# Kernel optimization log

Measured on AMD Instinct MI355X. Metric: run time of the kernel, lower is better.

Reference implementation:

```python
import jax, jax.numpy as jnp
import numpy as np

N_NODES = 50000
N_EDGES = 800000
N_GRAPHS = 512
IN_DIM, HID_DIM, EMB_DIM = 128, 256, 128
EPS = 1e-5


def setup_inputs() -> dict:
    key = jax.random.key(0)
    ks = jax.random.split(key, 12)
    x = jax.random.normal(ks[0], (N_NODES, IN_DIM), dtype=jnp.float32)
    edge_index = jax.random.randint(ks[1], (2, N_EDGES), 0, N_NODES, dtype=jnp.int32)
    batch = jnp.sort(jax.random.randint(ks[2], (N_NODES,), 0, N_GRAPHS, dtype=jnp.int32))
    s1 = 1.0 / np.sqrt(IN_DIM)
    s2 = 1.0 / np.sqrt(HID_DIM)
    return {
        "x": x,
        "edge_index": edge_index,
        "batch": batch,
        "W1": jax.random.uniform(ks[3], (IN_DIM, HID_DIM), jnp.float32, -s1, s1),
        "b1": jnp.zeros((HID_DIM,), jnp.float32),
        "gamma1": jnp.ones((HID_DIM,), jnp.float32),
        "beta1": jnp.zeros((HID_DIM,), jnp.float32),
        "W2": jax.random.uniform(ks[4], (HID_DIM, EMB_DIM), jnp.float32, -s2, s2),
        "b2": jnp.zeros((EMB_DIM,), jnp.float32),
        "gamma2": jnp.ones((EMB_DIM,), jnp.float32),
        "beta2": jnp.zeros((EMB_DIM,), jnp.float32),
    }


def _gcn_conv(x, W, b, src, dst, n_nodes):
    # PyG GCNConv: h = xW; aggregate with sym-normalized adjacency incl. self-loops; + bias
    h = x @ W  # [N, D]
    ones = jnp.ones(src.shape[0], dtype=h.dtype)
    deg = jax.ops.segment_sum(ones, dst, num_segments=n_nodes) + 1.0  # self-loop
    dinv = jax.lax.rsqrt(deg)
    norm = dinv[src] * dinv[dst]  # [E]
    msg = h[src] * norm[:, None]  # gather + scale  [E, D]
    agg = jax.ops.segment_sum(msg, dst, num_segments=n_nodes)
    agg = agg + h * (1.0 / deg)[:, None]  # self-loop contribution (norm = 1/deg)
    return agg + b


def _batchnorm(h, gamma, beta):
    mean = jnp.mean(h, axis=0)
    var = jnp.mean(jnp.square(h - mean), axis=0)  # biased, training mode
    return gamma * (h - mean) * jax.lax.rsqrt(var + EPS) + beta


def reference(x, edge_index, batch, W1, b1, gamma1, beta1, W2, b2, gamma2, beta2):
    src, dst = edge_index[0], edge_index[1]
    n = x.shape[0]
    h = _gcn_conv(x, W1, b1, src, dst, n)
    h = _batchnorm(jax.nn.relu(h), gamma1, beta1)
    h = _gcn_conv(h, W2, b2, src, dst, n)
    h = _batchnorm(jax.nn.relu(h), gamma2, beta2)
    return jax.ops.segment_max(h, batch, num_segments=N_GRAPHS)
```

## Files before the change

### kernel.cpp

```cpp
#include <hip/hip_runtime.h>
#include <math.h>

#define N_NODES 50000
#define N_EDGES 800000
#define N_GRAPHS 512
#define IN_DIM 128
#define HID_DIM 256
#define EMB_DIM 128
#define EPS 1e-5f
#define ELLW 64
#define NGROUP 8
#define GROUPN 6250
#define BLK_PER_GROUP 256
#define EPB ((N_EDGES + BLK_PER_GROUP - 1) / BLK_PER_GROUP)
#define F2B_N (N_NODES * IN_DIM / 4)
#define F2B_BLOCKS ((F2B_N + 255) / 256)
#define TW1_BLOCKS ((HID_DIM * IN_DIM + 255) / 256)
#define DINV_BLOCKS ((N_NODES + 255) / 256)

typedef __attribute__((ext_vector_type(8))) short bf16x8;
typedef __attribute__((ext_vector_type(4))) float f32x4;

static __device__ __forceinline__ unsigned short f2b(float f) {
    unsigned u = __float_as_uint(f);
    return (unsigned short)((u + 0x7fffu + ((u >> 16) & 1u)) >> 16);
}
static __device__ __forceinline__ float b2f(unsigned short h) {
    return __uint_as_float(((unsigned)h) << 16);
}

__global__ void __launch_bounds__(256) scatter_xcd(const int* __restrict__ src,
                                                   const int* __restrict__ dst,
                                                   int* __restrict__ fill,
                                                   int* __restrict__ col) {
    int b = blockIdx.x;
    int g = b & 7;
    int bs = b >> 3;
    int lo = g * GROUPN;
    int hi = lo + GROUPN;
    int e_end = min((bs + 1) * EPB, N_EDGES);
    for (int e = bs * EPB + threadIdx.x; e < e_end; e += 256) {
        int d = dst[e];
        if (d >= lo && d < hi) {
            int pos = atomicAdd(&fill[d], 1);
            pos = min(pos, ELLW - 1);
            col[(d << 6) + pos] = src[e];
        }
    }
}

__global__ void convert_kernel(const float* __restrict__ x, unsigned short* __restrict__ xbf,
                               const float* __restrict__ W1, unsigned short* __restrict__ W1t,
                               const int* __restrict__ fill, float* __restrict__ dinv) {
    int b = blockIdx.x;
    if (b < F2B_BLOCKS) {
        int i = b * 256 + threadIdx.x;
        if (i < F2B_N) {
            float4 v = ((const float4*)x)[i];
            ushort4 o;
            o.x = f2b(v.x); o.y = f2b(v.y); o.z = f2b(v.z); o.w = f2b(v.w);
            ((ushort4*)xbf)[i] = o;
        }
    } else if (b < F2B_BLOCKS + TW1_BLOCKS) {
        int j = (b - F2B_BLOCKS) * 256 + threadIdx.x;
        if (j < HID_DIM * IN_DIM) {
            int n = j >> 7;
            int k = j & 127;
            W1t[j] = f2b(W1[k * HID_DIM + n]);
        }
    } else {
        int v = (b - F2B_BLOCKS - TW1_BLOCKS) * 256 + threadIdx.x;
        if (v < N_NODES) dinv[v] = rsqrtf((float)(min(fill[v], ELLW) + 1));
    }
}

static __device__ __forceinline__ void acc8(float* acc, uint4 r, float w) {
    const unsigned* u = (const unsigned*)&r;
#pragma unroll
    for (int k = 0; k < 4; ++k) {
        float lo = __uint_as_float((u[k] & 0xFFFFu) << 16);
        float hi = __uint_as_float(u[k] & 0xFFFF0000u);
        acc[2 * k]     += w * lo;
        acc[2 * k + 1] += w * hi;
    }
}

template <bool RELU, bool OUT_BF, bool BIAS>
__global__ void __launch_bounds__(256) aggw_kernel(const unsigned short* __restrict__ h,
                                                   const float* __restrict__ dinv,
                                                   const int* __restrict__ deg,
                                                   const int* __restrict__ col,
                                                   const float* __restrict__ bias,
                                                   void* __restrict__ y) {
    int tid = threadIdx.x;
    int lane = tid & 63;
    int wid = tid >> 6;
    int v = blockIdx.x * 4 + wid;
    int g = lane >> 4;
    int p = lane & 15;

    int beg = v << 6;
    int end = beg + min(deg[v], ELLW);
    float acc[8] = {};

    for (int e = beg; e < end; e += 16) {
        int i0 = e + g, i1 = e + 4 + g, i2 = e + 8 + g, i3 = e + 12 + g;
        int c0 = min(i0, end - 1), c1 = min(i1, end - 1);
        int c2 = min(i2, end - 1), c3 = min(i3, end - 1);
        int u0 = col[c0], u1 = col[c1], u2 = col[c2], u3 = col[c3];
        float w0 = (i0 < end) ? dinv[u0] : 0.f;
        float w1 = (i1 < end) ? dinv[u1] : 0.f;
        float w2 = (i2 < end) ? dinv[u2] : 0.f;
        float w3 = (i3 < end) ? dinv[u3] : 0.f;
        uint4 d0 = *(const uint4*)(h + (size_t)u0 * 128 + p * 8);
        uint4 d1 = *(const uint4*)(h + (size_t)u1 * 128 + p * 8);
        uint4 d2 = *(const uint4*)(h + (size_t)u2 * 128 + p * 8);
        uint4 d3 = *(const uint4*)(h + (size_t)u3 * 128 + p * 8);
        acc8(acc, d0, w0);
        acc8(acc, d1, w1);
        acc8(acc, d2, w2);
        acc8(acc, d3, w3);
    }

#pragma unroll
    for (int k = 0; k < 8; ++k) {
        float a = acc[k];
        a += __shfl_xor(a, 16, 64);
        a += __shfl_xor(a, 32, 64);
        acc[k] = a;
    }

    if (g == 0) {
        uint4 selfr = *(const uint4*)(h + (size_t)v * 128 + p * 8);
        const unsigned* su = (const unsigned*)&selfr;
        float dv = dinv[v];
        float dv2 = dv * dv;
        float o[8];
#pragma unroll
        for (int k = 0; k < 4; ++k) {
            float lo = __uint_as_float((su[k] & 0xFFFFu) << 16);
            float hi = __uint_as_float(su[k] & 0xFFFF0000u);
            o[2 * k]     = dv * acc[2 * k]     + lo * dv2;
            o[2 * k + 1] = dv * acc[2 * k + 1] + hi * dv2;
        }
        if (BIAS) {
            float4 bv0 = *(const float4*)&bias[p * 8];
            float4 bv1 = *(const float4*)&bias[p * 8 + 4];
            o[0] += bv0.x; o[1] += bv0.y; o[2] += bv0.z; o[3] += bv0.w;
            o[4] += bv1.x; o[5] += bv1.y; o[6] += bv1.z; o[7] += bv1.w;
        }
        if (RELU) {
#pragma unroll
            for (int k = 0; k < 8; ++k) o[k] = fmaxf(o[k], 0.f);
        }
        if (OUT_BF) {
            uint4 packed;
            unsigned* pu = (unsigned*)&packed;
#pragma unroll
            for (int k = 0; k < 4; ++k)
                pu[k] = (unsigned)f2b(o[2 * k]) | ((unsigned)f2b(o[2 * k + 1]) << 16);
            *(uint4*)((unsigned short*)y + (size_t)v * 128 + p * 8) = packed;
        } else {
            float* yf = (float*)y + (size_t)v * 128 + p * 8;
            *(float4*)yf = make_float4(o[0], o[1], o[2], o[3]);
            *(float4*)(yf + 4) = make_float4(o[4], o[5], o[6], o[7]);
        }
    }
}

template <bool RELU, bool STATS>
__global__ void __launch_bounds__(256) mfma_gemm_kernel(const unsigned short* __restrict__ A,
                                                        const unsigned short* __restrict__ Bt,
                                                        const float* __restrict__ bias,
                                                        unsigned short* __restrict__ C,
                                                        float* __restrict__ sum,
                                                        float* __restrict__ sumsq,
                                                        int M, int N, int K) {
    const int LDT = 40;
    __shared__ unsigned short As[64 * LDT];
    __shared__ unsigned short Bs[128 * LDT];
    int tid = threadIdx.x;
    int bm = blockIdx.x * 64;
    int bn = blockIdx.y * 128;
    int lr = tid >> 2;
    int lc = (tid & 3) * 8;
    int lane = tid & 63;
    int w = tid >> 6;
    int wc = w * 32;
    int l15 = lane & 15, q = lane >> 4;

    f32x4 acc[4][2] = {};
    bool arow_ok = (bm + lr) < M;
    const unsigned short* Aptr = A + (size_t)(bm + lr) * K + lc;
    const unsigned short* B0 = Bt + (size_t)(bn + lr) * K + lc;
    const unsigned short* B1 = Bt + (size_t)(bn + lr + 64) * K + lc;

    for (int k0 = 0; k0 < K; k0 += 32) {
        uint4 av = arow_ok ? *(const uint4*)(Aptr + k0) : make_uint4(0u, 0u, 0u, 0u);
        uint4 b0v = *(const uint4*)(B0 + k0);
        uint4 b1v = *(const uint4*)(B1 + k0);
        *(uint4*)&As[lr * LDT + lc] = av;
        *(uint4*)&Bs[lr * LDT + lc] = b0v;
        *(uint4*)&Bs[(lr + 64) * LDT + lc] = b1v;
        __syncthreads();
        bf16x8 af[4], bf[2];
#pragma unroll
        for (int mi = 0; mi < 4; ++mi)
            af[mi] = *(const bf16x8*)&As[(mi * 16 + l15) * LDT + q * 8];
#pragma unroll
        for (int ni = 0; ni < 2; ++ni)
            bf[ni] = *(const bf16x8*)&Bs[(wc + ni * 16 + l15) * LDT + q * 8];
#pragma unroll
        for (int mi = 0; mi < 4; ++mi)
#pragma unroll
            for (int ni = 0; ni < 2; ++ni)
                acc[mi][ni] = __builtin_amdgcn_mfma_f32_16x16x32_bf16(af[mi], bf[ni], acc[mi][ni], 0, 0, 0);
        __syncthreads();
    }

    float s[2] = {0.f, 0.f}, sq[2] = {0.f, 0.f};
#pragma unroll
    for (int ni = 0; ni < 2; ++ni) {
        int colc = bn + wc + ni * 16 + l15;
        float bv = bias ? bias[colc] : 0.f;
#pragma unroll
        for (int mi = 0; mi < 4; ++mi) {
#pragma unroll
            for (int r = 0; r < 4; ++r) {
                int row = bm + mi * 16 + q * 4 + r;
                bool ok = row < M;
                float vv = acc[mi][ni][r] + bv;
                if (RELU) vv = fmaxf(vv, 0.f);
                unsigned short us = f2b(vv);
                if (ok) C[(size_t)row * N + colc] = us;
                if (STATS) {
                    float xr = ok ? b2f(us) : 0.f;
                    s[ni] += xr;
                    sq[ni] += xr * xr;
                }
            }
        }
    }
    if (STATS) {
#pragma unroll
        for (int ni = 0; ni < 2; ++ni) {
            float a = s[ni], b = sq[ni];
            a += __shfl_xor(a, 16, 64); a += __shfl_xor(a, 32, 64);
            b += __shfl_xor(b, 16, 64); b += __shfl_xor(b, 32, 64);
            if (q == 0) {
                int colc = bn + wc + ni * 16 + l15;
                atomicAdd(&sum[colc], a);
                atomicAdd(&sumsq[colc], b);
            }
        }
    }
}

template <int C, bool BF>
__global__ void __launch_bounds__(256) stats_fast(const void* __restrict__ yv,
                                                  float* __restrict__ sum,
                                                  float* __restrict__ sumsq) {
    constexpr int VEC = BF ? 8 : 4;
    constexpr int NCHUNK = C / VEC;
    constexpr int ROWS = 256 / NCHUNK;
    constexpr int STRIDE = 256 * ROWS;
    __shared__ float sp[256 * VEC];
    __shared__ float qp[256 * VEC];
    int t = threadIdx.x;
    int j = t & (NCHUNK - 1);
    float s[VEC], q[VEC];
#pragma unroll
    for (int k = 0; k < VEC; ++k) { s[k] = 0.f; q[k] = 0.f; }

    const char* base = (const char*)yv + (size_t)j * 16;
    auto body = [&](int v) {
        uint4 raw = *(const uint4*)(base + (size_t)v * (C * (BF ? 2 : 4)));
        float x[VEC];
        if (BF) {
            const unsigned* u = (const unsigned*)&raw;
#pragma unroll
            for (int k = 0; k < 4; ++k) {
                x[2 * k]     = __uint_as_float((u[k] & 0xFFFFu) << 16);
                x[2 * k + 1] = __uint_as_float(u[k] & 0xFFFF0000u);
            }
        } else {
            const float* f = (const float*)&raw;
#pragma unroll
            for (int k = 0; k < VEC; ++k) x[k] = f[k];
        }
#pragma unroll
        for (int k = 0; k < VEC; ++k) { s[k] += x[k]; q[k] += x[k] * x[k]; }
    };

    int v = blockIdx.x * ROWS + (t >> 5);
    for (; v + 3 * STRIDE < N_NODES; v += 4 * STRIDE) {
        body(v); body(v + STRIDE); body(v + 2 * STRIDE); body(v + 3 * STRIDE);
    }
    for (; v < N_NODES; v += STRIDE) body(v);

#pragma unroll
    for (int k = 0; k < VEC; ++k) { sp[t * VEC + k] = s[k]; qp[t * VEC + k] = q[k]; }
    __syncthreads();
    if (t < C) {
        float ss = 0.f, qq = 0.f;
#pragma unroll
        for (int rr = 0; rr < ROWS; ++rr) {
            ss += sp[rr * (NCHUNK * VEC) + t];
            qq += qp[rr * (NCHUNK * VEC) + t];
        }
        atomicAdd(&sum[t], ss);
        atomicAdd(&sumsq[t], qq);
    }
}

__global__ void prep2_kernel(const float* __restrict__ sum1, const float* __restrict__ sumsq1,
                             const float* __restrict__ gamma1, const float* __restrict__ beta1,
                             const float* __restrict__ W2, unsigned short* __restrict__ W2pt,
                             float* __restrict__ bc2) {
    __shared__ float a1s[HID_DIM], s1s[HID_DIM];
    int t = threadIdx.x;
    {
        float m = sum1[t] * (1.f / N_NODES);
        float var = sumsq1[t] * (1.f / N_NODES) - m * m;
        float a = gamma1[t] * rsqrtf(var + EPS);
        a1s[t] = a;
        s1s[t] = beta1[t] - m * a;
    }
    __syncthreads();
    if (t < EMB_DIM) {
        float bacc = 0.f;
        for (int k = 0; k < HID_DIM; ++k) {
            float w = W2[k * EMB_DIM + t];
            W2pt[t * HID_DIM + k] = f2b(a1s[k] * w);
            bacc += s1s[k] * w;
        }
        bc2[t] = bacc;
    }
}

__global__ void __launch_bounds__(128) segmax_kernel(const float* __restrict__ y,
                                                     const float* __restrict__ sum2,
                                                     const float* __restrict__ sumsq2,
                                                     const float* __restrict__ gamma2,
                                                     const float* __restrict__ beta2,
                                                     const int* __restrict__ batch,
                                                     float* __restrict__ out) {
    __shared__ int sh[2];
    int g = blockIdx.x;
    int c = threadIdx.x;
    float mch = sum2[c] * (1.f / N_NODES);
    float var = sumsq2[c] * (1.f / N_NODES) - mch * mch;
    float ac = gamma2[c] * rsqrtf(var + EPS);
    float sc = beta2[c] - mch * ac;
    if (threadIdx.x == 0) {
        int lo = 0, hi = N_NODES;
        while (lo < hi) { int mid = (lo + hi) >> 1; if (batch[mid] < g) lo = mid + 1; else hi = mid; }
        sh[0] = lo;
        hi = N_NODES;
        while (lo < hi) { int mid = (lo + hi) >> 1; if (batch[mid] < g + 1) lo = mid + 1; else hi = mid; }
        sh[1] = lo;
    }
    __syncthreads();
    int beg = sh[0], end = sh[1];
    float m = -INFINITY;
    for (int v = beg; v < end; ++v) {
        m = fmaxf(m, fmaf(ac, y[(size_t)v * EMB_DIM + c], sc));
    }
    out[(size_t)g * EMB_DIM + c] = m;
}

extern "C" void kernel_launch(void* const* d_in, const int* in_sizes, int n_in,
                              void* d_out, int out_size, void* d_ws, size_t ws_size,
                              hipStream_t stream) {
    const float* x      = (const float*)d_in[0];
    const int*   ei     = (const int*)d_in[1];
    const int*   batch  = (const int*)d_in[2];
    const float* W1     = (const float*)d_in[3];
    const float* b1     = (const float*)d_in[4];
    const float* gamma1 = (const float*)d_in[5];
    const float* beta1  = (const float*)d_in[6];
    const float* W2     = (const float*)d_in[7];
    const float* b2     = (const float*)d_in[8];
    const float* gamma2 = (const float*)d_in[9];
    const float* beta2  = (const float*)d_in[10];
    float* out = (float*)d_out;

    char* ws = (char*)d_ws;
    size_t off = 0;
    auto alloc = [&](size_t bytes) -> char* {
        char* p = ws + off;
        off = (off + bytes + 255) & ~(size_t)255;
        return p;
    };
    int*   fill   = (int*)alloc((size_t)N_NODES * 4);
    float* stats  = (float*)alloc(1024 * 4);
    size_t zbytes = off;
    int*   col    = (int*)alloc((size_t)N_NODES * ELLW * 4);
    float* dinv   = (float*)alloc((size_t)N_NODES * 4);
    float* bc2    = (float*)alloc((size_t)EMB_DIM * 4);
    unsigned short* W1t  = (unsigned short*)alloc((size_t)HID_DIM * IN_DIM * 2);
    unsigned short* W2pt = (unsigned short*)alloc((size_t)HID_DIM * EMB_DIM * 2);
    unsigned short* xbf  = (unsigned short*)alloc((size_t)N_NODES * IN_DIM * 2);
    unsigned short* axbf = (unsigned short*)alloc((size_t)N_NODES * IN_DIM * 2);
    unsigned short* y1bf = (unsigned short*)alloc((size_t)N_NODES * HID_DIM * 2);
    unsigned short* gbf  = (unsigned short*)alloc((size_t)N_NODES * EMB_DIM * 2);
    float* y2 = (float*)xbf;
    (void)ws_size; (void)in_sizes; (void)n_in; (void)out_size;

    const int* src  = ei;
    const int* dstp = ei + N_EDGES;

    hipMemsetAsync(ws, 0, zbytes, stream);

    scatter_xcd<<<NGROUP * BLK_PER_GROUP, 256, 0, stream>>>(src, dstp, fill, col);
    convert_kernel<<<F2B_BLOCKS + TW1_BLOCKS + DINV_BLOCKS, 256, 0, stream>>>(
        x, xbf, W1, W1t, fill, dinv);

    aggw_kernel<false, true, false><<<N_NODES / 4, 256, 0, stream>>>(xbf, dinv, fill, col, nullptr, axbf);
    dim3 g1((N_NODES + 63) / 64, HID_DIM / 128);
    mfma_gemm_kernel<true, true><<<g1, 256, 0, stream>>>(axbf, W1t, b1, y1bf,
                                                         stats, stats + 256,
                                                         N_NODES, HID_DIM, IN_DIM);

    prep2_kernel<<<1, 256, 0, stream>>>(stats, stats + 256, gamma1, beta1, W2, W2pt, bc2);

    dim3 g2((N_NODES + 63) / 64, EMB_DIM / 128);
    mfma_gemm_kernel<false, false><<<g2, 256, 0, stream>>>(y1bf, W2pt, bc2, gbf,
                                                           nullptr, nullptr,
                                                           N_NODES, EMB_DIM, HID_DIM);
    aggw_kernel<true, false, true><<<N_NODES / 4, 256, 0, stream>>>(gbf, dinv, fill, col, b2, y2);
    stats_fast<EMB_DIM, false><<<256, 256, 0, stream>>>(y2, stats + 512, stats + 640);

    segmax_kernel<<<N_GRAPHS, 128, 0, stream>>>(y2, stats + 512, stats + 640,
                                                gamma2, beta2, batch, out);
}
```

Measured before the change: 319.0 us.

## Keep whole weight matrix resident in LDS and A rows in registers for GEMMs

Replaces the tiled 64x128 MFMA GEMM, which staged A and B tiles through shared memory every 32-wide K step behind two barriers, with a kernel that loads the full transposed weight matrix once per block into LDS in MFMA-fragment order. Each wave keeps its 32 A rows entirely in registers and loops over all output column tiles. This removes per-K-step syncs and the re-reads of A across column blocks. In exchange it uses 64 KB of LDS per block, which limits occupancy, and many registers for the A fragments. Output stores remain scalar 2-byte writes.

```diff
diff --git a/kernel.cpp b/kernel.cpp
--- a/kernel.cpp
+++ b/kernel.cpp
@@ -17,6 +17,7 @@
 #define F2B_BLOCKS ((F2B_N + 255) / 256)
 #define TW1_BLOCKS ((HID_DIM * IN_DIM + 255) / 256)
 #define DINV_BLOCKS ((N_NODES + 255) / 256)
+#define GEMM_BLOCKS ((N_NODES + 127) / 128)
 
 typedef __attribute__((ext_vector_type(8))) short bf16x8;
 typedef __attribute__((ext_vector_type(4))) float f32x4;
@@ -168,89 +169,90 @@
     }
 }
 
-template <bool RELU, bool STATS>
-__global__ void __launch_bounds__(256) mfma_gemm_kernel(const unsigned short* __restrict__ A,
-                                                        const unsigned short* __restrict__ Bt,
-                                                        const float* __restrict__ bias,
-                                                        unsigned short* __restrict__ C,
-                                                        float* __restrict__ sum,
-                                                        float* __restrict__ sumsq,
-                                                        int M, int N, int K) {
-    const int LDT = 40;
-    __shared__ unsigned short As[64 * LDT];
-    __shared__ unsigned short Bs[128 * LDT];
+template <bool RELU, bool STATS, int N, int K>
+__global__ void __launch_bounds__(256) gemm_wres(const unsigned short* __restrict__ A,
+                                                 const unsigned short* __restrict__ Bt,
+                                                 const float* __restrict__ bias,
+                                                 unsigned short* __restrict__ C,
+                                                 float* __restrict__ sum,
+                                                 float* __restrict__ sumsq,
+                                                 int M) {
+    constexpr int NT = N / 16;
+    constexpr int KT = K / 32;
+    __shared__ unsigned short Blds[N * K];
     int tid = threadIdx.x;
-    int bm = blockIdx.x * 64;
-    int bn = blockIdx.y * 128;
-    int lr = tid >> 2;
-    int lc = (tid & 3) * 8;
     int lane = tid & 63;
     int w = tid >> 6;
-    int wc = w * 32;
     int l15 = lane & 15, q = lane >> 4;
 
-    f32x4 acc[4][2] = {};
-    bool arow_ok = (bm + lr) < M;
-    const unsigned short* Aptr = A + (size_t)(bm + lr) * K + lc;
-    const unsigned short* B0 = Bt + (size_t)(bn + lr) * K + lc;
-    const unsigned short* B1 = Bt + (size_t)(bn + lr + 64) * K + lc;
-
-    for (int k0 = 0; k0 < K; k0 += 32) {
-        uint4 av = arow_ok ? *(const uint4*)(Aptr + k0) : make_uint4(0u, 0u, 0u, 0u);
-        uint4 b0v = *(const uint4*)(B0 + k0);
-        uint4 b1v = *(const uint4*)(B1 + k0);
-        *(uint4*)&As[lr * LDT + lc] = av;
-        *(uint4*)&Bs[lr * LDT + lc] = b0v;
-        *(uint4*)&Bs[(lr + 64) * LDT + lc] = b1v;
-        __syncthreads();
-        bf16x8 af[4], bf[2];
-#pragma unroll
-        for (int mi = 0; mi < 4; ++mi)
-            af[mi] = *(const bf16x8*)&As[(mi * 16 + l15) * LDT + q * 8];
-#pragma unroll
-        for (int ni = 0; ni < 2; ++ni)
-            bf[ni] = *(const bf16x8*)&Bs[(wc + ni * 16 + l15) * LDT + q * 8];
-#pragma unroll
-        for (int mi = 0; mi < 4; ++mi)
-#pragma unroll
-            for (int ni = 0; ni < 2; ++ni)
-                acc[mi][ni] = __builtin_amdgcn_mfma_f32_16x16x32_bf16(af[mi], bf[ni], acc[mi][ni], 0, 0, 0);
-        __syncthreads();
-    }
-
-    float s[2] = {0.f, 0.f}, sq[2] = {0.f, 0.f};
-#pragma unroll
-    for (int ni = 0; ni < 2; ++ni) {
-        int colc = bn + wc + ni * 16 + l15;
-        float bv = bias ? bias[colc] : 0.f;
-#pragma unroll
-        for (int mi = 0; mi < 4; ++mi) {
-#pragma unroll
-            for (int r = 0; r < 4; ++r) {
-                int row = bm + mi * 16 + q * 4 + r;
-                bool ok = row < M;
-                float vv = acc[mi][ni][r] + bv;
-                if (RELU) vv = fmaxf(vv, 0.f);
-                unsigned short us = f2b(vv);
-                if (ok) C[(size_t)row * N + colc] = us;
-                if (STATS) {
-                    float xr = ok ? b2f(us) : 0.f;
-                    s[ni] += xr;
-                    sq[ni] += xr * xr;
+    for (int c = tid; c < N * K / 8; c += 256) {
+        int f = c >> 6;
+        int l = c & 63;
+        int nt = f / KT, kk = f - nt * KT;
+        int sl15 = l & 15, sq = l >> 4;
+        uint4 v = *(const uint4*)(Bt + (size_t)(nt * 16 + sl15) * K + kk * 32 + sq * 8);
+        *(uint4*)&Blds[(size_t)c * 8] = v;
+    }
+    __syncthreads();
+
+    int mbase = blockIdx.x * 128 + w * 32;
+    int ar0 = mbase + l15;
+    int ar1 = mbase + 16 + l15;
+    int ac0 = min(ar0, M - 1);
+    int ac1 = min(ar1, M - 1);
+
+    uint4 areg0[KT], areg1[KT];
+#pragma unroll
+    for (int kk = 0; kk < KT; ++kk) {
+        areg0[kk] = *(const uint4*)(A + (size_t)ac0 * K + kk * 32 + q * 8);
+        areg1[kk] = *(const uint4*)(A + (size_t)ac1 * K + kk * 32 + q * 8);
+    }
+
+    for (int nt = 0; nt < NT; nt += 2) {
+        f32x4 acc00 = {}, acc01 = {}, acc10 = {}, acc11 = {};
+#pragma unroll
+        for (int kk = 0; kk < KT; ++kk) {
+            bf16x8 b0 = *(const bf16x8*)&Blds[(size_t)(((nt + 0) * KT + kk) * 64 + lane) * 8];
+            bf16x8 b1 = *(const bf16x8*)&Blds[(size_t)(((nt + 1) * KT + kk) * 64 + lane) * 8];
+            bf16x8 a0 = *(const bf16x8*)&areg0[kk];
+            bf16x8 a1 = *(const bf16x8*)&areg1[kk];
+            acc00 = __builtin_amdgcn_mfma_f32_16x16x32_bf16(a0, b0, acc00, 0, 0, 0);
+            acc10 = __builtin_amdgcn_mfma_f32_16x16x32_bf16(a1, b0, acc10, 0, 0, 0);
+            acc01 = __builtin_amdgcn_mfma_f32_16x16x32_bf16(a0, b1, acc01, 0, 0, 0);
+            acc11 = __builtin_amdgcn_mfma_f32_16x16x32_bf16(a1, b1, acc11, 0, 0, 0);
+        }
+#pragma unroll
+        for (int ni = 0; ni < 2; ++ni) {
+            int colc = (nt + ni) * 16 + l15;
+            float bv = bias ? bias[colc] : 0.f;
+            float s = 0.f, sq2 = 0.f;
+#pragma unroll
+            for (int mi = 0; mi < 2; ++mi) {
+                const f32x4& acc = (mi == 0) ? (ni == 0 ? acc00 : acc01)
+                                             : (ni == 0 ? acc10 : acc11);
+                int rbase = mbase + mi * 16 + q * 4;
+#pragma unroll
+                for (int r = 0; r < 4; ++r) {
+                    int row = rbase + r;
+                    bool ok = row < M;
+                    float vv = acc[r] + bv;
+                    if (RELU) vv = fmaxf(vv, 0.f);
+                    unsigned short us = f2b(vv);
+                    if (ok) C[(size_t)row * N + colc] = us;
+                    if (STATS) {
+                        float xr = ok ? b2f(us) : 0.f;
+                        s += xr;
+                        sq2 += xr * xr;
+                    }
                 }
             }
-        }
-    }
-    if (STATS) {
-#pragma unroll
-        for (int ni = 0; ni < 2; ++ni) {
-            float a = s[ni], b = sq[ni];
-            a += __shfl_xor(a, 16, 64); a += __shfl_xor(a, 32, 64);
-            b += __shfl_xor(b, 16, 64); b += __shfl_xor(b, 32, 64);
-            if (q == 0) {
-                int colc = bn + wc + ni * 16 + l15;
-                atomicAdd(&sum[colc], a);
-                atomicAdd(&sumsq[colc], b);
+            if (STATS) {
+                s += __shfl_xor(s, 16, 64);  s += __shfl_xor(s, 32, 64);
+                sq2 += __shfl_xor(sq2, 16, 64); sq2 += __shfl_xor(sq2, 32, 64);
+                if (q == 0) {
+                    atomicAdd(&sum[colc], s);
+                    atomicAdd(&sumsq[colc], sq2);
+                }
             }
         }
     }
@@ -417,17 +419,13 @@
         x, xbf, W1, W1t, fill, dinv);
 
     aggw_kernel<false, true, false><<<N_NODES / 4, 256, 0, stream>>>(xbf, dinv, fill, col, nullptr, axbf);
-    dim3 g1((N_NODES + 63) / 64, HID_DIM / 128);
-    mfma_gemm_kernel<true, true><<<g1, 256, 0, stream>>>(axbf, W1t, b1, y1bf,
-                                                         stats, stats + 256,
-                                                         N_NODES, HID_DIM, IN_DIM);
+    gemm_wres<true, true, HID_DIM, IN_DIM><<<GEMM_BLOCKS, 256, 0, stream>>>(
+        axbf, W1t, b1, y1bf, stats, stats + 256, N_NODES);
 
     prep2_kernel<<<1, 256, 0, stream>>>(stats, stats + 256, gamma1, beta1, W2, W2pt, bc2);
 
-    dim3 g2((N_NODES + 63) / 64, EMB_DIM / 128);
-    mfma_gemm_kernel<false, false><<<g2, 256, 0, stream>>>(y1bf, W2pt, bc2, gbf,
-                                                           nullptr, nullptr,
-                                                           N_NODES, EMB_DIM, HID_DIM);
+    gemm_wres<false, false, EMB_DIM, HID_DIM><<<GEMM_BLOCKS, 256, 0, stream>>>(
+        y1bf, W2pt, bc2, gbf, nullptr, nullptr, N_NODES);
     aggw_kernel<true, false, true><<<N_NODES / 4, 256, 0, stream>>>(gbf, dinv, fill, col, b2, y2);
     stats_fast<EMB_DIM, false><<<256, 256, 0, stream>>>(y2, stats + 512, stats + 640);
 
```

New measurement: 391.3 us. +22.7%, slower.
